# Kernel optimization log

Hardware: AMD Instinct MI355X
Metric: run time of the kernel (lower is better)

The kernel has to match this reference:

```python
import jax, jax.numpy as jnp
import numpy as np

NH = 4; HD = 128; C = 512; GRID = 14; L = GRID * GRID  # 196 tokens

def _rel_index():
    ch = np.arange(GRID)
    coords = np.stack(np.meshgrid(ch, ch, indexing='ij')).reshape(2, -1)  # [2, L_grid]
    rel = (coords[:, :, None] - coords[:, None, :]).transpose(1, 2, 0).copy()  # [L,L,2]
    rel[:, :, 0] += GRID - 1
    rel[:, :, 1] += GRID - 1
    rel[:, :, 0] *= 2 * GRID - 1
    return rel.sum(-1)  # [L,L] in [0, (2*GRID-1)^2)

REL_IDX = jnp.asarray(_rel_index())

def _pool7(x):
    # exact adaptive_avg_pool2d to (7,7): H,W are multiples of 7
    B, Cc, H, W = x.shape
    return x.reshape(B, Cc, 7, H // 7, 7, W // 7).mean(axis=(3, 5))

def _ln(x, g, b):
    m = x.mean(-1, keepdims=True)
    v = ((x - m) ** 2).mean(-1, keepdims=True)
    return (x - m) / jnp.sqrt(v + 1e-5) * g + b

def _attn(x, qkv_w, qkv_b, bt, pw, pb):
    B, Lx, Cx = x.shape
    qkv = (x @ qkv_w + qkv_b).reshape(B, Lx, 3, NH, HD).transpose(2, 0, 3, 1, 4)
    q, k, v = qkv[0] * (HD ** -0.5), qkv[1], qkv[2]  # [B,NH,L,HD]
    attn = jnp.einsum('bhld,bhmd->bhlm', q, k)
    bias = bt[REL_IDX]  # gather: [L,L,NH]
    attn = jax.nn.softmax(attn + bias.transpose(2, 0, 1)[None], axis=-1)
    o = jnp.einsum('bhlm,bhmd->bhld', attn, v).transpose(0, 2, 1, 3).reshape(B, Lx, Cx)
    return o @ pw + pb

def _layer(x, ln1_g, ln1_b, qkv_w, qkv_b, bt, pw, pb, ln2_g, ln2_b, w1, b1, w2, b2):
    x = x + _attn(_ln(x, ln1_g, ln1_b), qkv_w, qkv_b, bt, pw, pb)
    h = _ln(x, ln2_g, ln2_b)
    return x + jax.nn.relu(h @ w1 + b1) @ w2 + b2


def setup_inputs() -> dict:
    key = jax.random.key(0)
    ks = iter(jax.random.split(key, 40))
    chans = [96, 192, 384, 768]
    sizes = [56, 28, 14, 7]
    B = 64
    d = {}
    for i, (c, s) in enumerate(zip(chans, sizes)):
        d[f'feat{i}'] = jax.random.normal(next(ks), (B, c, s, s), jnp.float32)
    for i, c in enumerate(chans):
        d[f'proj_w{i}'] = jax.random.normal(next(ks), (C, c), jnp.float32) * 0.02
        d[f'proj_b{i}'] = jnp.zeros((C,), jnp.float32)
    NL = 2
    d['ln1_g'] = jnp.ones((NL, C)); d['ln1_b'] = jnp.zeros((NL, C))
    d['qkv_w'] = jax.random.normal(next(ks), (NL, C, 3 * C), jnp.float32) * 0.02
    d['qkv_b'] = jnp.zeros((NL, 3 * C))
    d['bias_table'] = jax.random.normal(next(ks), (NL, (2 * GRID - 1) ** 2, NH), jnp.float32) * 0.02
    d['attn_pw'] = jax.random.normal(next(ks), (NL, C, C), jnp.float32) * 0.02
    d['attn_pb'] = jnp.zeros((NL, C))
    d['ln2_g'] = jnp.ones((NL, C)); d['ln2_b'] = jnp.zeros((NL, C))
    d['mlp_w1'] = jax.random.normal(next(ks), (NL, C, 4 * C), jnp.float32) * 0.02
    d['mlp_b1'] = jnp.zeros((NL, 4 * C))
    d['mlp_w2'] = jax.random.normal(next(ks), (NL, 4 * C, C), jnp.float32) * 0.02
    d['mlp_b2'] = jnp.zeros((NL, C))
    return d


def reference(feat0, feat1, feat2, feat3,
              proj_w0, proj_b0, proj_w1, proj_b1, proj_w2, proj_b2, proj_w3, proj_b3,
              ln1_g, ln1_b, qkv_w, qkv_b, bias_table, attn_pw, attn_pb,
              ln2_g, ln2_b, mlp_w1, mlp_b1, mlp_w2, mlp_b2):
    feats = [feat0, feat1, feat2, feat3]
    pws = [proj_w0, proj_w1, proj_w2, proj_w3]
    pbs = [proj_b0, proj_b1, proj_b2, proj_b3]
    tokens = []
    for f, w, b in zip(feats, pws, pbs):
        p = _pool7(f)  # [B,Cin,7,7]
        t = jnp.einsum('bchw,oc->bhwo', p, w) + b  # 1x1 conv -> channels-last
        tokens.append(t.reshape(t.shape[0], 49, C))
    x = jnp.concatenate(tokens, axis=1)  # [B,196,512]
    for l in range(ln1_g.shape[0]):
        x = _layer(x, ln1_g[l], ln1_b[l], qkv_w[l], qkv_b[l], bias_table[l],
                   attn_pw[l], attn_pb[l], ln2_g[l], ln2_b[l],
                   mlp_w1[l], mlp_b1[l], mlp_w2[l], mlp_b2[l])
    return x.mean(axis=1)  # [B,512]
```

## Files before the change

kernel.cpp:

```cpp
#include <hip/hip_runtime.h>
#include <hip/hip_bf16.h>

typedef __attribute__((ext_vector_type(8))) short short8;
typedef __attribute__((ext_vector_type(4))) float f32x4;

__device__ __forceinline__ unsigned short f2bf(float x) {
    unsigned int u = __builtin_bit_cast(unsigned int, x);
    unsigned int r = (u + 0x7FFFu + ((u >> 16) & 1u)) >> 16;
    return (unsigned short)r;
}

__device__ __forceinline__ void gload_lds16(const unsigned short* g, unsigned short* l) {
    __builtin_amdgcn_global_load_lds(
        (const __attribute__((address_space(1))) unsigned int*)g,
        (__attribute__((address_space(3))) unsigned int*)l, 16, 0, 0);
}

__global__ __launch_bounds__(256) void gemm64(
    const unsigned short* __restrict__ A, int lda,
    const unsigned short* __restrict__ B, int ldb,
    void* __restrict__ Cv, int ldc,
    const float* __restrict__ bias,
    const float* __restrict__ res, int ldres,
    int K, int relu, int mode,
    unsigned short* q_out, unsigned short* k_out, unsigned short* v_out,
    float qscale)
{
    int bx = blockIdx.x, by = blockIdx.y;
    {
        const int gx = gridDim.x;
        const int total = gx * gridDim.y;
        if ((total & 7) == 0) {
            const int orig = by * gx + bx;
            const int per = total >> 3;
            const int nf = (orig & 7) * per + (orig >> 3);
            bx = nf % gx;
            by = nf / gx;
        }
    }
    const int bm = by * 128;
    const int bn = bx * 128;

    __shared__ unsigned short As[2][128][64];
    __shared__ unsigned short Bs[2][128][64];

    const int tid  = threadIdx.x;
    const int lane = tid & 63;
    const int wid  = tid >> 6;
    const int wm   = wid >> 1;
    const int wn   = wid & 1;
    const int slot = lane >> 4;
    const int lcol = lane & 15;

    const int trow = tid >> 3;
    const int tgrn = tid & 7;
    const int scol_dst = tgrn * 8;
    const int scol_src = (tgrn ^ (trow & 7)) * 8;

    const unsigned short* pa[4];
    const unsigned short* pb[4];
    #pragma unroll
    for (int p = 0; p < 4; ++p) {
        pa[p] = A + (long long)(bm + p * 32 + trow) * lda + scol_src;
        pb[p] = B + (long long)(bn + p * 32 + trow) * ldb + scol_src;
    }

    f32x4 acc[4][4];
    #pragma unroll
    for (int i = 0; i < 4; ++i)
        #pragma unroll
        for (int j = 0; j < 4; ++j)
            acc[i][j] = (f32x4){0.f, 0.f, 0.f, 0.f};

    const int nt = K >> 6;

    #pragma unroll
    for (int p = 0; p < 4; ++p) {
        gload_lds16(pa[p], &As[0][p * 32 + trow][scol_dst]);
        gload_lds16(pb[p], &Bs[0][p * 32 + trow][scol_dst]);
    }
    __syncthreads();

    for (int t = 0; t < nt; ++t) {
        const int cur = t & 1;
        if (t + 1 < nt) {
            const int nb = (t + 1) & 1;
            const long long koff = (long long)(t + 1) << 6;
            #pragma unroll
            for (int p = 0; p < 4; ++p) {
                gload_lds16(pa[p] + koff, &As[nb][p * 32 + trow][scol_dst]);
                gload_lds16(pb[p] + koff, &Bs[nb][p * 32 + trow][scol_dst]);
            }
        }

        short8 afr[4][2], bfr[4][2];
        #pragma unroll
        for (int mi = 0; mi < 4; ++mi) {
            const int row = wm * 64 + mi * 16 + lcol;
            #pragma unroll
            for (int ks = 0; ks < 2; ++ks) {
                const int g = ((ks * 4 + slot) ^ (lcol & 7)) * 8;
                afr[mi][ks] = *(const short8*)&As[cur][row][g];
            }
        }
        #pragma unroll
        for (int ni = 0; ni < 4; ++ni) {
            const int row = wn * 64 + ni * 16 + lcol;
            #pragma unroll
            for (int ks = 0; ks < 2; ++ks) {
                const int g = ((ks * 4 + slot) ^ (lcol & 7)) * 8;
                bfr[ni][ks] = *(const short8*)&Bs[cur][row][g];
            }
        }
        #pragma unroll
        for (int mi = 0; mi < 4; ++mi)
            #pragma unroll
            for (int ni = 0; ni < 4; ++ni)
                #pragma unroll
                for (int ks = 0; ks < 2; ++ks)
                    acc[mi][ni] = __builtin_amdgcn_mfma_f32_16x16x32_bf16(
                        afr[mi][ks], bfr[ni][ks], acc[mi][ni], 0, 0, 0);

        __syncthreads();
    }

    float* Cf = (float*)Cv;
    unsigned short* Cb = (unsigned short*)Cv;

    #pragma unroll
    for (int mi = 0; mi < 4; ++mi) {
        int rbase = bm + wm * 64 + mi * 16 + slot * 4;
        #pragma unroll
        for (int ni = 0; ni < 4; ++ni) {
            int gc = bn + wn * 64 + ni * 16 + lcol;
            float bv = bias ? bias[gc] : 0.f;
            f32x4 a = acc[mi][ni];
            #pragma unroll
            for (int rr = 0; rr < 4; ++rr) {
                int gr = rbase + rr;
                float v = a[rr] + bv;
                if (mode == 0) {
                    if (res) v += res[(long long)gr * ldres + gc];
                    if (relu) v = fmaxf(v, 0.f);
                    Cf[(long long)gr * ldc + gc] = v;
                } else if (mode == 2) {
                    int which = gc >> 9;
                    int hh = (gc >> 7) & 3;
                    int d  = gc & 127;
                    int b_ = gr / 196, l_ = gr % 196;
                    int zz = b_ * 4 + hh;
                    if (which == 0)
                        q_out[((long long)zz * 196 + l_) * 128 + d] = f2bf(v * qscale);
                    else if (which == 1)
                        k_out[((long long)zz * 196 + l_) * 128 + d] = f2bf(v);
                    else
                        v_out[((long long)zz * 128 + d) * 224 + l_] = f2bf(v);
                } else {
                    if (relu) v = fmaxf(v, 0.f);
                    Cb[(long long)gr * ldc + gc] = f2bf(v);
                }
            }
        }
    }
}

__global__ __launch_bounds__(256) void gemm_bf16(
    const unsigned short* __restrict__ A, long long sA, int lda,
    const unsigned short* __restrict__ B, long long sB, int ldb,
    void* __restrict__ Cv, long long sC, int ldc,
    const float* __restrict__ bias,
    const float* __restrict__ res, int ldres,
    int M, int N, int K,
    int relu, int mode, int rowoff,
    unsigned short* q_out, unsigned short* k_out, unsigned short* v_out,
    float qscale)
{
    const int z = blockIdx.z;
    A += (long long)z * sA;
    B += (long long)z * sB;

    const int bm = blockIdx.y * 128;
    const int bn = blockIdx.x * 128;

    __shared__ unsigned short As[3][128][32];
    __shared__ unsigned short Bs[3][128][32];

    const int tid  = threadIdx.x;
    const int lane = tid & 63;
    const int wid  = tid >> 6;
    const int wm   = wid >> 1;
    const int wn   = wid & 1;
    const int slot = lane >> 4;
    const int lcol = lane & 15;

    const int srow = tid >> 2;
    const int sgrn = tid & 3;
    const int scol_dst = sgrn * 8;
    const int scol_src = (sgrn ^ ((srow >> 1) & 3)) * 8;
    const int rslot = (slot ^ ((lcol >> 1) & 3)) * 8;

    int ga0 = bm + srow;       if (ga0 > M - 1) ga0 = M - 1;
    int ga1 = bm + 64 + srow;  if (ga1 > M - 1) ga1 = M - 1;
    int gb0 = bn + srow;       if (gb0 > N - 1) gb0 = N - 1;
    int gb1 = bn + 64 + srow;  if (gb1 > N - 1) gb1 = N - 1;
    const unsigned short* pa0 = A + (long long)ga0 * lda + scol_src;
    const unsigned short* pa1 = A + (long long)ga1 * lda + scol_src;
    const unsigned short* pb0 = B + (long long)gb0 * ldb + scol_src;
    const unsigned short* pb1 = B + (long long)gb1 * ldb + scol_src;

    f32x4 acc[4][4];
    #pragma unroll
    for (int i = 0; i < 4; ++i)
        #pragma unroll
        for (int j = 0; j < 4; ++j)
            acc[i][j] = (f32x4){0.f, 0.f, 0.f, 0.f};

    const int nt = K >> 5;

    gload_lds16(pa0, &As[0][srow][scol_dst]);
    gload_lds16(pa1, &As[0][64 + srow][scol_dst]);
    gload_lds16(pb0, &Bs[0][srow][scol_dst]);
    gload_lds16(pb1, &Bs[0][64 + srow][scol_dst]);
    if (nt > 1) {
        gload_lds16(pa0 + 32, &As[1][srow][scol_dst]);
        gload_lds16(pa1 + 32, &As[1][64 + srow][scol_dst]);
        gload_lds16(pb0 + 32, &Bs[1][srow][scol_dst]);
        gload_lds16(pb1 + 32, &Bs[1][64 + srow][scol_dst]);
    }

    int cur = 0;
    for (int t = 0; t < nt; ++t) {
        const int nxt2 = t + 2;
        if (nxt2 < nt) {
            const int nb = nxt2 % 3;
            const long long koff = (long long)nxt2 << 5;
            gload_lds16(pa0 + koff, &As[nb][srow][scol_dst]);
            gload_lds16(pa1 + koff, &As[nb][64 + srow][scol_dst]);
            gload_lds16(pb0 + koff, &Bs[nb][srow][scol_dst]);
            gload_lds16(pb1 + koff, &Bs[nb][64 + srow][scol_dst]);
        }
        if (nxt2 < nt)          asm volatile("s_waitcnt vmcnt(8)" ::: "memory");
        else if (t + 1 < nt)    asm volatile("s_waitcnt vmcnt(4)" ::: "memory");
        else                    asm volatile("s_waitcnt vmcnt(0)" ::: "memory");
        __builtin_amdgcn_s_barrier();
        __builtin_amdgcn_sched_barrier(0);

        short8 afr[4], bfr[4];
        #pragma unroll
        for (int mi = 0; mi < 4; ++mi)
            afr[mi] = *(const short8*)&As[cur][wm * 64 + mi * 16 + lcol][rslot];
        #pragma unroll
        for (int ni = 0; ni < 4; ++ni)
            bfr[ni] = *(const short8*)&Bs[cur][wn * 64 + ni * 16 + lcol][rslot];
        #pragma unroll
        for (int mi = 0; mi < 4; ++mi)
            #pragma unroll
            for (int ni = 0; ni < 4; ++ni)
                acc[mi][ni] = __builtin_amdgcn_mfma_f32_16x16x32_bf16(
                    afr[mi], bfr[ni], acc[mi][ni], 0, 0, 0);

        __builtin_amdgcn_s_barrier();
        cur = (cur == 2) ? 0 : cur + 1;
    }

    float* Cf = (float*)Cv + (mode == 0 ? (long long)z * sC : 0);

    #pragma unroll
    for (int mi = 0; mi < 4; ++mi) {
        int rbase = bm + wm * 64 + mi * 16 + slot * 4;
        #pragma unroll
        for (int ni = 0; ni < 4; ++ni) {
            int gc = bn + wn * 64 + ni * 16 + lcol;
            if (gc >= N) continue;
            float bv = bias ? bias[gc] : 0.f;
            f32x4 a = acc[mi][ni];
            #pragma unroll
            for (int rr = 0; rr < 4; ++rr) {
                int gr = rbase + rr;
                if (gr >= M) continue;
                float v = a[rr] + bv;
                if (mode == 0) {
                    if (res) v += res[(long long)gr * ldres + gc];
                    if (relu) v = fmaxf(v, 0.f);
                    Cf[(long long)gr * ldc + gc] = v;
                } else {
                    int orow = (gr / 49) * 196 + rowoff + (gr % 49);
                    Cf[(long long)orow * ldc + gc] = v;
                }
            }
        }
    }
}

__global__ __launch_bounds__(256) void flash_k(
    const unsigned short* __restrict__ q_bf,
    const unsigned short* __restrict__ k_bf,
    const unsigned short* __restrict__ v_t,
    unsigned short* __restrict__ O,
    const float* __restrict__ bt)
{
    const int z = blockIdx.x;
    const int h = z & 3, bb = z >> 2;
    const int tid = threadIdx.x;
    const int w = tid >> 6;
    const int lane = tid & 63;
    const int slot = lane >> 4;
    const int lcol = lane & 15;

    __shared__ unsigned short Ps[4][16][68];

    const unsigned short* Qz = q_bf + (long long)z * 196 * 128;
    const unsigned short* Kz = k_bf + (long long)z * 196 * 128;
    const unsigned short* Vz = v_t  + (long long)z * 128 * 224;

    short8 qf[4][4];
    #pragma unroll
    for (int i = 0; i < 4; ++i) {
        const int row = (w + 4 * i) * 16 + lcol;
        #pragma unroll
        for (int ks = 0; ks < 4; ++ks)
            qf[i][ks] = *(const short8*)(Qz + (long long)row * 128 + ks * 32 + slot * 8);
    }

    f32x4 o[4][8];
    #pragma unroll
    for (int i = 0; i < 4; ++i)
        #pragma unroll
        for (int nd = 0; nd < 8; ++nd)
            o[i][nd] = (f32x4){0.f, 0.f, 0.f, 0.f};

    float m_r[4][4], l_r[4][4];
    #pragma unroll
    for (int i = 0; i < 4; ++i)
        #pragma unroll
        for (int r = 0; r < 4; ++r) { m_r[i][r] = -3e38f; l_r[i][r] = 0.f; }

    int qi1[4][4], qj1[4][4];
    #pragma unroll
    for (int i = 0; i < 4; ++i)
        #pragma unroll
        for (int r = 0; r < 4; ++r) {
            int q = (w + 4 * i) * 16 + slot * 4 + r;
            int qq = q < 195 ? q : 195;
            qi1[i][r] = qq / 14;
            qj1[i][r] = qq % 14;
        }

    #pragma unroll
    for (int kt = 0; kt < 4; ++kt) {
        const int nkj  = (kt == 3) ? 2 : 4;
        const int nksl = (kt == 3) ? 1 : 2;

        short8 kf[4][4];
        #pragma unroll
        for (int kj = 0; kj < 4; ++kj) {
            if (kj >= nkj) continue;
            const int krow = kt * 64 + kj * 16 + lcol;
            #pragma unroll
            for (int ks = 0; ks < 4; ++ks)
                kf[kj][ks] = *(const short8*)(Kz + (long long)krow * 128 + ks * 32 + slot * 8);
        }

        f32x4 s[4][4];
        __builtin_amdgcn_s_setprio(1);
        #pragma unroll
        for (int i = 0; i < 4; ++i)
            #pragma unroll
            for (int kj = 0; kj < 4; ++kj) {
                if (kj >= nkj) continue;
                f32x4 a = (f32x4){0.f, 0.f, 0.f, 0.f};
                #pragma unroll
                for (int ks = 0; ks < 4; ++ks)
                    a = __builtin_amdgcn_mfma_f32_16x16x32_bf16(qf[i][ks], kf[kj][ks], a, 0, 0, 0);
                s[i][kj] = a;
            }
        __builtin_amdgcn_s_setprio(0);

        short8 vf[8][2];
        #pragma unroll
        for (int nd = 0; nd < 8; ++nd)
            #pragma unroll
            for (int ksl = 0; ksl < 2; ++ksl) {
                if (ksl >= nksl) continue;
                vf[nd][ksl] = *(const short8*)(Vz + (long long)(nd * 16 + lcol) * 224
                                               + kt * 64 + ksl * 32 + slot * 8);
            }

        #pragma unroll
        for (int i = 0; i < 4; ++i) {
            #pragma unroll
            for (int kj = 0; kj < 4; ++kj) {
                if (kj >= nkj) continue;
                const int key = kt * 64 + kj * 16 + lcol;
                const int kk = key < 195 ? key : 195;
                const int i2 = kk / 14, j2 = kk % 14;
                #pragma unroll
                for (int r = 0; r < 4; ++r) {
                    const int idx = (qi1[i][r] - i2 + 13) * 27 + (qj1[i][r] - j2 + 13);
                    float sv = s[i][kj][r] + bt[idx * 4 + h];
                    if (key >= 196) sv = -3e38f;
                    s[i][kj][r] = sv;
                }
            }
            f32x4 pm = s[i][0];
            #pragma unroll
            for (int kj = 1; kj < 4; ++kj) {
                if (kj >= nkj) continue;
                #pragma unroll
                for (int r = 0; r < 4; ++r) pm[r] = fmaxf(pm[r], s[i][kj][r]);
            }
            #pragma unroll
            for (int r = 0; r < 4; ++r) {
                #pragma unroll
                for (int off = 1; off < 16; off <<= 1)
                    pm[r] = fmaxf(pm[r], __shfl_xor(pm[r], off));
            }
            float sf[4];
            #pragma unroll
            for (int r = 0; r < 4; ++r) {
                float mn = fmaxf(m_r[i][r], pm[r]);
                sf[r] = __expf(m_r[i][r] - mn);
                m_r[i][r] = mn;
            }
            f32x4 ladd = (f32x4){0.f, 0.f, 0.f, 0.f};
            #pragma unroll
            for (int kj = 0; kj < 4; ++kj) {
                if (kj >= nkj) continue;
                #pragma unroll
                for (int r = 0; r < 4; ++r) {
                    float p = __expf(s[i][kj][r] - m_r[i][r]);
                    s[i][kj][r] = p;
                    ladd[r] += p;
                }
            }
            #pragma unroll
            for (int r = 0; r < 4; ++r) {
                #pragma unroll
                for (int off = 1; off < 16; off <<= 1)
                    ladd[r] += __shfl_xor(ladd[r], off);
                l_r[i][r] = l_r[i][r] * sf[r] + ladd[r];
            }
            #pragma unroll
            for (int nd = 0; nd < 8; ++nd)
                #pragma unroll
                for (int r = 0; r < 4; ++r) o[i][nd][r] *= sf[r];
            #pragma unroll
            for (int kj = 0; kj < 4; ++kj) {
                if (kj >= nkj) continue;
                #pragma unroll
                for (int r = 0; r < 4; ++r)
                    Ps[w][slot * 4 + r][kj * 16 + lcol] = f2bf(s[i][kj][r]);
            }
            __builtin_amdgcn_s_setprio(1);
            #pragma unroll
            for (int ksl = 0; ksl < 2; ++ksl) {
                if (ksl >= nksl) continue;
                short8 pa = *(const short8*)&Ps[w][lcol][ksl * 32 + slot * 8];
                #pragma unroll
                for (int nd = 0; nd < 8; ++nd)
                    o[i][nd] = __builtin_amdgcn_mfma_f32_16x16x32_bf16(pa, vf[nd][ksl], o[i][nd], 0, 0, 0);
            }
            __builtin_amdgcn_s_setprio(0);
        }
    }

    #pragma unroll
    for (int i = 0; i < 4; ++i) {
        #pragma unroll
        for (int r = 0; r < 4; ++r) {
            const int q = (w + 4 * i) * 16 + slot * 4 + r;
            if (q >= 196) continue;
            const float rn = 1.f / l_r[i][r];
            unsigned short* op = O + ((long long)(bb * 196 + q)) * 512 + h * 128 + lcol;
            #pragma unroll
            for (int nd = 0; nd < 8; ++nd)
                op[nd * 16] = f2bf(o[i][nd][r] * rn);
        }
    }
}

__global__ __launch_bounds__(256) void wconv_t(const float* __restrict__ W,
                                               unsigned short* __restrict__ Wt,
                                               int K, int N)
{
    W  += (long long)blockIdx.z * K * N;
    Wt += (long long)blockIdx.z * K * N;
    __shared__ float t[32][33];
    int tx = threadIdx.x & 31, ty = threadIdx.x >> 5;
    int n0 = blockIdx.x * 32, k0 = blockIdx.y * 32;
    #pragma unroll
    for (int j = 0; j < 4; ++j)
        t[ty + j * 8][tx] = W[(long long)(k0 + ty + j * 8) * N + n0 + tx];
    __syncthreads();
    #pragma unroll
    for (int j = 0; j < 4; ++j)
        Wt[(long long)(n0 + ty + j * 8) * K + k0 + tx] = f2bf(t[tx][ty + j * 8]);
}

__global__ __launch_bounds__(256) void wcv_k(const float* __restrict__ in,
                                             unsigned short* __restrict__ out, int n)
{
    int i = blockIdx.x * 256 + threadIdx.x;
    if (i < n) out[i] = f2bf(in[i]);
}

template<int F>
__global__ __launch_bounds__(256) void pool_k(const float* __restrict__ feat,
                                              unsigned short* __restrict__ P, int ch)
{
    const int S = 7 * F;
    int wv = blockIdx.x * 4 + (threadIdx.x >> 6);
    int lane = threadIdx.x & 63;
    int b = wv / ch, c = wv % ch;
    if (lane >= 49) return;
    int oh = lane / 7, ow = lane % 7;
    const float* src = feat + ((long long)b * ch + c) * (S * S) + (oh * F) * S + ow * F;
    float acc = 0.f;
    #pragma unroll
    for (int hh = 0; hh < F; ++hh) {
        const float* row = src + hh * S;
        if constexpr (F == 8) {
            float4 a = *(const float4*)row;
            float4 d = *(const float4*)(row + 4);
            acc += a.x + a.y + a.z + a.w + d.x + d.y + d.z + d.w;
        } else if constexpr (F == 4) {
            float4 a = *(const float4*)row;
            acc += a.x + a.y + a.z + a.w;
        } else if constexpr (F == 2) {
            float2 a = *(const float2*)row;
            acc += a.x + a.y;
        } else {
            acc += row[0];
        }
    }
    P[((long long)(b * 49 + lane)) * ch + c] = f2bf(acc * (1.f / (F * F)));
}

__global__ __launch_bounds__(256) void ln_k(const float* __restrict__ x,
                                            unsigned short* __restrict__ y,
                                            const float* __restrict__ g,
                                            const float* __restrict__ b)
{
    long long row = blockIdx.x * 4 + (threadIdx.x >> 6);
    const float* xr = x + row * 512;
    unsigned short* yr = y + row * 512;
    int lane = threadIdx.x & 63;
    float v[8];
    float s = 0.f, ss = 0.f;
    #pragma unroll
    for (int p = 0; p < 8; ++p) {
        v[p] = xr[lane + p * 64];
        s += v[p]; ss += v[p] * v[p];
    }
    #pragma unroll
    for (int off = 32; off >= 1; off >>= 1) {
        s  += __shfl_xor(s, off);
        ss += __shfl_xor(ss, off);
    }
    float mean = s * (1.f / 512.f);
    float var  = ss * (1.f / 512.f) - mean * mean;
    float rstd = rsqrtf(var + 1e-5f);
    #pragma unroll
    for (int p = 0; p < 8; ++p) {
        int c = lane + p * 64;
        yr[c] = f2bf((v[p] - mean) * rstd * g[c] + b[c]);
    }
}

__global__ __launch_bounds__(512) void mean_k(const float* __restrict__ X,
                                              float* __restrict__ out)
{
    int b = blockIdx.x, c = threadIdx.x;
    const float* xp = X + (long long)b * 196 * 512 + c;
    float s = 0.f;
    for (int t = 0; t < 196; ++t) s += xp[t * 512];
    out[b * 512 + c] = s * (1.f / 196.f);
}

extern "C" void kernel_launch(void* const* d_in, const int* in_sizes, int n_in,
                              void* d_out, int out_size, void* d_ws, size_t ws_size,
                              hipStream_t stream)
{
    const float* feat[4]   = {(const float*)d_in[0], (const float*)d_in[1],
                              (const float*)d_in[2], (const float*)d_in[3]};
    const float* proj_w[4] = {(const float*)d_in[4], (const float*)d_in[6],
                              (const float*)d_in[8], (const float*)d_in[10]};
    const float* proj_b[4] = {(const float*)d_in[5], (const float*)d_in[7],
                              (const float*)d_in[9], (const float*)d_in[11]};
    const float* ln1_g = (const float*)d_in[12];
    const float* ln1_b = (const float*)d_in[13];
    const float* qkv_w = (const float*)d_in[14];
    const float* qkv_b = (const float*)d_in[15];
    const float* bias_table = (const float*)d_in[16];
    const float* attn_pw = (const float*)d_in[17];
    const float* attn_pb = (const float*)d_in[18];
    const float* ln2_g = (const float*)d_in[19];
    const float* ln2_b = (const float*)d_in[20];
    const float* mlp_w1 = (const float*)d_in[21];
    const float* mlp_b1 = (const float*)d_in[22];
    const float* mlp_w2 = (const float*)d_in[23];
    const float* mlp_b2 = (const float*)d_in[24];

    const long long NXT = 64LL * 196 * 512;

    float* X  = (float*)d_ws;
    float* S  = X + NXT;
    unsigned short* O_bf = (unsigned short*)S;

    unsigned short* ub    = (unsigned short*)(S + 256LL * 196 * 196);
    unsigned short* XN_bf = ub;
    unsigned short* q_bf  = XN_bf + NXT;
    unsigned short* k_bf  = q_bf + NXT;
    unsigned short* v_t   = k_bf + NXT;
    unsigned short* H     = q_bf;
    unsigned short* wts   = v_t + 256LL * 128 * 224 + 256LL * 196 * 224;

    unsigned short* qkvw_t = wts;
    unsigned short* pw_t   = qkvw_t + 2LL * 1536 * 512;
    unsigned short* w1_t   = pw_t   + 2LL * 512 * 512;
    unsigned short* w2_t   = w1_t   + 2LL * 2048 * 512;
    unsigned short* pjw    = w2_t   + 2LL * 512 * 2048;
    unsigned short* P_bf   = pjw + 512LL * (96 + 192 + 384 + 768);
    unsigned short* pjw_i[4];
    const int chans[4] = {96, 192, 384, 768};
    {
        unsigned short* p = pjw;
        for (int i = 0; i < 4; ++i) { pjw_i[i] = p; p += 512LL * chans[i]; }
    }

    wconv_t<<<dim3(1536/32, 512/32, 2), 256, 0, stream>>>(qkv_w, qkvw_t, 512, 1536);
    wconv_t<<<dim3(512/32, 512/32, 2), 256, 0, stream>>>(attn_pw, pw_t, 512, 512);
    wconv_t<<<dim3(2048/32, 512/32, 2), 256, 0, stream>>>(mlp_w1, w1_t, 512, 2048);
    wconv_t<<<dim3(512/32, 2048/32, 2), 256, 0, stream>>>(mlp_w2, w2_t, 2048, 512);
    for (int i = 0; i < 4; ++i) {
        int n = 512 * chans[i];
        wcv_k<<<(n + 255) / 256, 256, 0, stream>>>(proj_w[i], pjw_i[i], n);
    }

    pool_k<8><<<64 * 96  / 4, 256, 0, stream>>>(feat[0], P_bf, 96);
    gemm_bf16<<<dim3(4, 25, 1), 256, 0, stream>>>(
        P_bf, 0, 96, pjw_i[0], 0, 96, X, 0, 512, proj_b[0], nullptr, 0,
        3136, 512, 96, 0, 1, 0, nullptr, nullptr, nullptr, 0.f);
    pool_k<4><<<64 * 192 / 4, 256, 0, stream>>>(feat[1], P_bf, 192);
    gemm_bf16<<<dim3(4, 25, 1), 256, 0, stream>>>(
        P_bf, 0, 192, pjw_i[1], 0, 192, X, 0, 512, proj_b[1], nullptr, 0,
        3136, 512, 192, 0, 1, 49, nullptr, nullptr, nullptr, 0.f);
    pool_k<2><<<64 * 384 / 4, 256, 0, stream>>>(feat[2], P_bf, 384);
    gemm_bf16<<<dim3(4, 25, 1), 256, 0, stream>>>(
        P_bf, 0, 384, pjw_i[2], 0, 384, X, 0, 512, proj_b[2], nullptr, 0,
        3136, 512, 384, 0, 1, 98, nullptr, nullptr, nullptr, 0.f);
    pool_k<1><<<64 * 768 / 4, 256, 0, stream>>>(feat[3], P_bf, 768);
    gemm_bf16<<<dim3(4, 25, 1), 256, 0, stream>>>(
        P_bf, 0, 768, pjw_i[3], 0, 768, X, 0, 512, proj_b[3], nullptr, 0,
        3136, 512, 768, 0, 1, 147, nullptr, nullptr, nullptr, 0.f);

    for (int l = 0; l < 2; ++l) {
        ln_k<<<3136, 256, 0, stream>>>(X, XN_bf, ln1_g + l * 512, ln1_b + l * 512);

        gemm64<<<dim3(12, 98), 256, 0, stream>>>(
            XN_bf, 512,
            qkvw_t + (long long)l * 1536 * 512, 512,
            nullptr, 0,
            qkv_b + l * 1536, nullptr, 0,
            512, 0, 2,
            q_bf, k_bf, v_t, 0.08838834764831845f);

        flash_k<<<256, 256, 0, stream>>>(q_bf, k_bf, v_t, O_bf,
                                         bias_table + (long long)l * 729 * 4);

        gemm64<<<dim3(4, 98), 256, 0, stream>>>(
            O_bf, 512,
            pw_t + (long long)l * 512 * 512, 512,
            X, 512,
            attn_pb + l * 512, X, 512,
            512, 0, 0,
            nullptr, nullptr, nullptr, 0.f);

        ln_k<<<3136, 256, 0, stream>>>(X, XN_bf, ln2_g + l * 512, ln2_b + l * 512);

        gemm64<<<dim3(16, 98), 256, 0, stream>>>(
            XN_bf, 512,
            w1_t + (long long)l * 2048 * 512, 512,
            H, 2048,
            mlp_b1 + l * 2048, nullptr, 0,
            512, 1, 4,
            nullptr, nullptr, nullptr, 0.f);

        gemm64<<<dim3(4, 98), 256, 0, stream>>>(
            H, 2048,
            w2_t + (long long)l * 512 * 2048, 2048,
            X, 512,
            mlp_b2 + l * 512, X, 512,
            2048, 0, 0,
            nullptr, nullptr, nullptr, 0.f);
    }

    mean_k<<<64, 512, 0, stream>>>(X, (float*)d_out);
}
```

Baseline: 762.5 us.

## Add 256x256-tile bf16 GEMM kernel for QKV and MLP-up projections

Adds a new 512-thread GEMM kernel that computes 256x256 output tiles, with double-buffered LDS filled by direct global-to-LDS loads, XOR-swizzled columns and XCD-aware block remapping. The QKV projection and the first MLP GEMM now use it instead of the 64-row kernel. Larger tiles are meant to raise data reuse per block and MFMA density and to cut global traffic. The cost is fewer blocks (294 and 392) on a large GPU, heavy register pressure from 32 accumulators per thread, and a mode 4 path that now always falls to the generic store.

```diff
diff --git a/kernel.cpp b/kernel.cpp
--- a/kernel.cpp
+++ b/kernel.cpp
@@ -14,6 +14,139 @@
     __builtin_amdgcn_global_load_lds(
         (const __attribute__((address_space(1))) unsigned int*)g,
         (__attribute__((address_space(3))) unsigned int*)l, 16, 0, 0);
+}
+
+__global__ __launch_bounds__(512)
+__attribute__((amdgpu_waves_per_eu(2, 2)))
+void gemm256b(
+    const unsigned short* __restrict__ A, int lda,
+    const unsigned short* __restrict__ B, int ldb,
+    void* __restrict__ Cv, int ldc,
+    const float* __restrict__ bias,
+    int K, int relu, int mode,
+    unsigned short* q_out, unsigned short* k_out, unsigned short* v_out,
+    float qscale)
+{
+    int bx = blockIdx.x, by = blockIdx.y;
+    {
+        const int gx = gridDim.x;
+        const int total = gx * gridDim.y;
+        const int orig = by * gx + bx;
+        const int q = total >> 3, r = total & 7;
+        const int xcd = orig & 7, idx = orig >> 3;
+        const int nf = (xcd < r ? xcd * (q + 1) : r * (q + 1) + (xcd - r) * q) + idx;
+        bx = nf % gx;
+        by = nf / gx;
+    }
+    const int bm = by * 256;
+    const int bn = bx * 256;
+
+    __shared__ unsigned short As[2][256][64];
+    __shared__ unsigned short Bs[2][256][64];
+
+    const int tid  = threadIdx.x;
+    const int lane = tid & 63;
+    const int wid  = tid >> 6;
+    const int wm   = wid >> 2;
+    const int wn   = wid & 3;
+    const int slot = lane >> 4;
+    const int lcol = lane & 15;
+
+    const int trow = tid >> 3;
+    const int tgrn = tid & 7;
+    const int scol_dst = tgrn * 8;
+    const int scol_src = (tgrn ^ (trow & 7)) * 8;
+
+    const unsigned short* pa[4];
+    const unsigned short* pb[4];
+    #pragma unroll
+    for (int p = 0; p < 4; ++p) {
+        pa[p] = A + (long long)(bm + p * 64 + trow) * lda + scol_src;
+        pb[p] = B + (long long)(bn + p * 64 + trow) * ldb + scol_src;
+    }
+
+    f32x4 acc[8][4];
+    #pragma unroll
+    for (int i = 0; i < 8; ++i)
+        #pragma unroll
+        for (int j = 0; j < 4; ++j)
+            acc[i][j] = (f32x4){0.f, 0.f, 0.f, 0.f};
+
+    const int nt = K >> 6;
+
+    #pragma unroll
+    for (int p = 0; p < 4; ++p) {
+        gload_lds16(pa[p], &As[0][p * 64 + trow][scol_dst]);
+        gload_lds16(pb[p], &Bs[0][p * 64 + trow][scol_dst]);
+    }
+    __syncthreads();
+
+    for (int t = 0; t < nt; ++t) {
+        const int cur = t & 1;
+        if (t + 1 < nt) {
+            const int nb = (t + 1) & 1;
+            const long long koff = (long long)(t + 1) << 6;
+            #pragma unroll
+            for (int p = 0; p < 4; ++p) {
+                gload_lds16(pa[p] + koff, &As[nb][p * 64 + trow][scol_dst]);
+                gload_lds16(pb[p] + koff, &Bs[nb][p * 64 + trow][scol_dst]);
+            }
+        }
+
+        #pragma unroll
+        for (int ks = 0; ks < 2; ++ks) {
+            const int g = ((ks * 4 + slot) ^ (lcol & 7)) * 8;
+            short8 afr[8], bfr[4];
+            #pragma unroll
+            for (int mi = 0; mi < 8; ++mi)
+                afr[mi] = *(const short8*)&As[cur][wm * 128 + mi * 16 + lcol][g];
+            #pragma unroll
+            for (int ni = 0; ni < 4; ++ni)
+                bfr[ni] = *(const short8*)&Bs[cur][wn * 64 + ni * 16 + lcol][g];
+            #pragma unroll
+            for (int mi = 0; mi < 8; ++mi)
+                #pragma unroll
+                for (int ni = 0; ni < 4; ++ni)
+                    acc[mi][ni] = __builtin_amdgcn_mfma_f32_16x16x32_bf16(
+                        afr[mi], bfr[ni], acc[mi][ni], 0, 0, 0);
+        }
+
+        __syncthreads();
+    }
+
+    unsigned short* Cb = (unsigned short*)Cv;
+
+    #pragma unroll
+    for (int mi = 0; mi < 8; ++mi) {
+        int rbase = bm + wm * 128 + mi * 16 + slot * 4;
+        #pragma unroll
+        for (int ni = 0; ni < 4; ++ni) {
+            int gc = bn + wn * 64 + ni * 16 + lcol;
+            float bv = bias ? bias[gc] : 0.f;
+            f32x4 a = acc[mi][ni];
+            #pragma unroll
+            for (int rr = 0; rr < 4; ++rr) {
+                int gr = rbase + rr;
+                float v = a[rr] + bv;
+                if (mode == 2) {
+                    int which = gc >> 9;
+                    int hh = (gc >> 7) & 3;
+                    int d  = gc & 127;
+                    int b_ = gr / 196, l_ = gr % 196;
+                    int zz = b_ * 4 + hh;
+                    if (which == 0)
+                        q_out[((long long)zz * 196 + l_) * 128 + d] = f2bf(v * qscale);
+                    else if (which == 1)
+                        k_out[((long long)zz * 196 + l_) * 128 + d] = f2bf(v);
+                    else
+                        v_out[((long long)zz * 128 + d) * 224 + l_] = f2bf(v);
+                } else {
+                    if (relu) v = fmaxf(v, 0.f);
+                    Cb[(long long)gr * ldc + gc] = f2bf(v);
+                }
+            }
+        }
+    }
 }
 
 __global__ __launch_bounds__(256) void gemm64(
@@ -657,11 +790,11 @@
     for (int l = 0; l < 2; ++l) {
         ln_k<<<3136, 256, 0, stream>>>(X, XN_bf, ln1_g + l * 512, ln1_b + l * 512);
 
-        gemm64<<<dim3(12, 98), 256, 0, stream>>>(
+        gemm256b<<<dim3(6, 49), 512, 0, stream>>>(
             XN_bf, 512,
             qkvw_t + (long long)l * 1536 * 512, 512,
             nullptr, 0,
-            qkv_b + l * 1536, nullptr, 0,
+            qkv_b + l * 1536,
             512, 0, 2,
             q_bf, k_bf, v_t, 0.08838834764831845f);
 
@@ -678,11 +811,11 @@
 
         ln_k<<<3136, 256, 0, stream>>>(X, XN_bf, ln2_g + l * 512, ln2_b + l * 512);
 
-        gemm64<<<dim3(16, 98), 256, 0, stream>>>(
+        gemm256b<<<dim3(8, 49), 512, 0, stream>>>(
             XN_bf, 512,
             w1_t + (long long)l * 2048 * 512, 512,
             H, 2048,
-            mlp_b1 + l * 2048, nullptr, 0,
+            mlp_b1 + l * 2048,
             512, 1, 4,
             nullptr, nullptr, nullptr, 0.f);
 
```

Measured after the change: 1.362 ms. 1.79x slower.
